# Optimization experiments

Hardware: AMD Instinct MI355X
Metric: run time of the kernel (lower is better)

The kernel has to match this reference:

```python
import jax, jax.numpy as jnp
import numpy as np

B, S, H, NH = 1, 4096, 768, 12
D = H // NH  # per-head dim = 64


def setup_inputs() -> dict:
    key = jax.random.key(0)
    ks = jax.random.split(key, 10)
    p = 0.02  # param scale
    return {
        "x": jax.random.normal(ks[0], (B, S, H), jnp.float32),
        "Wq": jax.random.normal(ks[1], (H, H), jnp.float32) * p,
        "bq": jax.random.normal(ks[2], (H,), jnp.float32) * p,
        "Wk": jax.random.normal(ks[3], (H, H), jnp.float32) * p,
        "bk": jax.random.normal(ks[4], (H,), jnp.float32) * p,
        "Wv": jax.random.normal(ks[5], (H, H), jnp.float32) * p,
        "bv": jax.random.normal(ks[6], (H,), jnp.float32) * p,
        "Wo": jax.random.normal(ks[7], (H, H), jnp.float32) * p,
        "bo": jax.random.normal(ks[8], (H,), jnp.float32) * p,
        "attn_mask": jax.random.randint(ks[9], (B, 1, 1, S), 0, 2).astype(bool),
    }


def _split_heads(t):
    # [B, S, H] -> [B, NH, S, D]
    return t.reshape(B, S, NH, D).transpose(0, 2, 1, 3)


def reference(x, Wq, bq, Wk, bk, Wv, bv, Wo, bo, attn_mask):
    q = _split_heads(x @ Wq.T + bq)
    k = _split_heads(x @ Wk.T + bk)
    v = _split_heads(x @ Wv.T + bv)
    scores = jnp.einsum('bhqd,bhkd->bhqk', q, k) / np.sqrt(D).astype(np.float32)
    scores = jnp.where(attn_mask, jnp.float32(-1e9), scores)
    attn = jax.nn.softmax(scores, axis=-1)
    ctx = jnp.einsum('bhqk,bhkd->bhqd', attn, v)
    ctx = ctx.transpose(0, 2, 1, 3).reshape(B, S, H)  # merge heads
    return ctx @ Wo.T + bo
```

## Files before the change

kernel.cpp:

```cpp
#include <hip/hip_runtime.h>
#include <stdint.h>

#define S_LEN 4096
#define HDIM  768
#define NHEAD 12
#define DHEAD 64

typedef _Float16 f16;
typedef __attribute__((ext_vector_type(8)))  _Float16 f16x8;
typedef __attribute__((ext_vector_type(4)))  _Float16 f16x4;
typedef __attribute__((ext_vector_type(4)))  float    f32x4;
typedef __attribute__((ext_vector_type(16))) float    f32x16;

typedef __attribute__((address_space(1))) void gv_t;
typedef __attribute__((address_space(3))) void lv_t;

__device__ __forceinline__ void async_copy16(const void* g, void* l) {
  __builtin_amdgcn_global_load_lds((gv_t*)g, (lv_t*)l, 16, 0, 0);
}

__device__ __forceinline__ float fast_exp2(float x) {
#if __has_builtin(__builtin_amdgcn_exp2f)
  return __builtin_amdgcn_exp2f(x);
#else
  return exp2f(x);
#endif
}

__device__ __forceinline__ int swz4(int row) { return (row ^ (row >> 2)) & 3; }

constexpr size_t OFF_META = 0;
constexpr size_t OFF_RIDX = 256;
constexpr size_t OFF_XB   = 65536;
constexpr size_t SZ_XB    = (size_t)S_LEN * HDIM * 2;
constexpr size_t OFF_WQKV = OFF_XB + SZ_XB;
constexpr size_t SZ_WQKV  = (size_t)3 * HDIM * HDIM * 2;
constexpr size_t OFF_WO   = OFF_WQKV + SZ_WQKV;
constexpr size_t SZ_WO    = (size_t)HDIM * HDIM * 2;
constexpr size_t OFF_Q    = OFF_WO + SZ_WO;
constexpr size_t SZ_HD    = (size_t)NHEAD * S_LEN * DHEAD * 2;
constexpr size_t OFF_K    = OFF_Q + SZ_HD;
constexpr size_t OFF_VT   = OFF_K + SZ_HD;
constexpr size_t OFF_VR   = OFF_VT + SZ_HD;
constexpr size_t OFF_PO1  = OFF_VR + SZ_HD;

__global__ __launch_bounds__(256) void k_prep(const float* __restrict__ x,
                                              const float* __restrict__ wq,
                                              const float* __restrict__ wk,
                                              const float* __restrict__ wv,
                                              const float* __restrict__ wo,
                                              const int* __restrict__ mi,
                                              f16* __restrict__ dst,
                                              int* __restrict__ ridx,
                                              int* __restrict__ meta) {
  __shared__ int s_flag;
  __shared__ int s_cnt[256];
  const int b = blockIdx.x, tid = threadIdx.x;
  if (b < 5376) {
    int i = b * 256 + tid;
    const float* src; int off;
    if (i < 786432) { src = x; off = i; }
    else {
      int j = i - 786432;
      int w = j / 147456;
      off = j - w * 147456;
      src = (w == 0) ? wq : (w == 1) ? wk : (w == 2) ? wv : wo;
    }
    float4 v = ((const float4*)src)[off];
    f16x4 h;
    h[0] = (f16)v.x; h[1] = (f16)v.y; h[2] = (f16)v.z; h[3] = (f16)v.w;
    ((f16x4*)dst)[i] = h;
    return;
  }
  if (tid == 0) s_flag = 1;
  __syncthreads();
  int bad = 0;
  #pragma unroll
  for (int k = 0; k < 4; ++k) {
    int v = mi[k * 256 + tid];
    if (v != 0 && v != 1) bad = 1;
  }
  if (bad) atomicAnd(&s_flag, 0);
  __syncthreads();
  const int isInt = s_flag;
  const unsigned char* mu8 = (const unsigned char*)mi;
  int keep[16]; int cnt = 0;
  const int s0 = tid * 16;
  #pragma unroll
  for (int k = 0; k < 16; ++k) {
    int mval = isInt ? mi[s0 + k] : (int)mu8[s0 + k];
    keep[k] = (mval == 0) ? 1 : 0;
    cnt += keep[k];
    ridx[s0 + k] = 0;
  }
  s_cnt[tid] = cnt;
  __syncthreads();
  for (int off = 1; off < 256; off <<= 1) {
    int t = (tid >= off) ? s_cnt[tid - off] : 0;
    __syncthreads();
    s_cnt[tid] += t;
    __syncthreads();
  }
  int base = s_cnt[tid] - cnt;
  #pragma unroll
  for (int k = 0; k < 16; ++k) {
    if (keep[k]) { ridx[base] = s0 + k; ++base; }
  }
  if (tid == 255) meta[0] = s_cnt[255];
}

__global__ __launch_bounds__(256) void k_qkv(
    const f16* __restrict__ xb, const f16* __restrict__ wqkv,
    const float* __restrict__ bq, const float* __restrict__ bk, const float* __restrict__ bv,
    const int* __restrict__ ridx, const int* __restrict__ meta,
    f16* __restrict__ Qh, f16* __restrict__ Kc, f16* __restrict__ Vrow) {
  __shared__ __attribute__((aligned(16))) f16 lA[128 * 32];
  __shared__ __attribute__((aligned(16))) f16 lB[128 * 32];
  const int tid = threadIdx.x;
  const int wid = tid >> 6, lane = tid & 63;
  const int hf = lane >> 5, l31 = lane & 31;
  const int wm = wid >> 1, wn = wid & 1;
  const int tn = blockIdx.x;
  const int m0 = blockIdx.y * 128;
  const int mat = tn / 6;
  const int nb = (tn % 6) * 128;
  const int kc = meta[0];
  if (mat != 0 && m0 >= kc) return;
  const f16* wbase = wqkv + (size_t)mat * HDIM * HDIM;

  const int ar0 = tid >> 2, ar1 = 64 + (tid >> 2);
  const f16* asrc0;
  const f16* asrc1;
  if (mat == 0) {
    asrc0 = xb + (size_t)(m0 + ar0) * HDIM;
    asrc1 = xb + (size_t)(m0 + ar1) * HDIM;
  } else {
    int g0 = (m0 + ar0 < kc) ? ridx[m0 + ar0] : 0;
    int g1 = (m0 + ar1 < kc) ? ridx[m0 + ar1] : 0;
    asrc0 = xb + (size_t)g0 * HDIM;
    asrc1 = xb + (size_t)g1 * HDIM;
  }
  const int slot = tid & 3;
  const int gs0 = slot ^ swz4(ar0);
  const int gs1 = slot ^ swz4(ar1);

  f32x16 acc[2][2] = {};

  for (int k0 = 0; k0 < HDIM; k0 += 32) {
    async_copy16((const char*)(asrc0 + k0) + gs0 * 16, (char*)lA + (wid * 64) * 16);
    async_copy16((const char*)(asrc1 + k0) + gs1 * 16, (char*)lA + (256 + wid * 64) * 16);
    async_copy16((const char*)(wbase + (size_t)(nb + ar0) * HDIM + k0) + gs0 * 16,
                 (char*)lB + (wid * 64) * 16);
    async_copy16((const char*)(wbase + (size_t)(nb + ar1) * HDIM + k0) + gs1 * 16,
                 (char*)lB + (256 + wid * 64) * 16);
    __syncthreads();
    #pragma unroll
    for (int kk = 0; kk < 2; ++kk) {
      f16x8 af[2], bf[2];
      #pragma unroll
      for (int mi = 0; mi < 2; ++mi) {
        int row = wm * 64 + mi * 32 + l31;
        af[mi] = *(const f16x8*)&lA[row * 32 + (((kk * 2 + hf) ^ swz4(row)) * 8)];
      }
      #pragma unroll
      for (int ni = 0; ni < 2; ++ni) {
        int row = wn * 64 + ni * 32 + l31;
        bf[ni] = *(const f16x8*)&lB[row * 32 + (((kk * 2 + hf) ^ swz4(row)) * 8)];
      }
      #pragma unroll
      for (int mi = 0; mi < 2; ++mi)
        #pragma unroll
        for (int ni = 0; ni < 2; ++ni)
          acc[mi][ni] = __builtin_amdgcn_mfma_f32_32x32x16_f16(af[mi], bf[ni], acc[mi][ni], 0, 0, 0);
    }
    __syncthreads();
  }

  const float* bias = (mat == 0) ? bq : (mat == 1) ? bk : bv;
  const float qscale = 0.125f * 1.44269504088896341f;
  f16* kvdst = (mat == 1) ? Kc : Vrow;
  #pragma unroll
  for (int mi = 0; mi < 2; ++mi) {
    #pragma unroll
    for (int ni = 0; ni < 2; ++ni) {
      int n = nb + wn * 64 + ni * 32 + l31;
      int head = n >> 6, d = n & 63;
      float b = bias[n];
      #pragma unroll
      for (int reg = 0; reg < 16; ++reg) {
        int s = m0 + wm * 64 + mi * 32 + (reg & 3) + 8 * (reg >> 2) + 4 * hf;
        float val = acc[mi][ni][reg] + b;
        if (mat == 0) {
          Qh[((size_t)head * S_LEN + s) * DHEAD + d] = (f16)(val * qscale);
        } else if (s < kc) {
          kvdst[((size_t)head * S_LEN + s) * DHEAD + d] = (f16)val;
        }
      }
    }
  }
}

__global__ __launch_bounds__(256) void k_vt(const int* __restrict__ meta,
                                            const f16* __restrict__ Vrow,
                                            f16* __restrict__ Vtc,
                                            f16* __restrict__ Kc) {
  const int kc = meta[0];
  const int kcp = (kc + 63) & ~63;
  const int p0 = blockIdx.x * 64;
  const int h = blockIdx.y;
  const int tid = threadIdx.x;
  if (p0 >= kcp) return;
  if (p0 <= kc && kc < p0 + 64 && kc < kcp) {
    const int npad = kcp - kc;
    for (int u = tid; u < npad * 8; u += 256) {
      int r = kc + (u >> 3), c8 = u & 7;
      f16x8 z = {};
      *(f16x8*)&Kc[((size_t)h * S_LEN + r) * DHEAD + c8 * 8] = z;
    }
  }
  __shared__ __attribute__((aligned(16))) f16 lT[64 * 80];
  for (int u = tid; u < 512; u += 256) {
    int d8 = u >> 6, p = u & 63;
    f16x8 v = {};
    if (p0 + p < kc) v = *(const f16x8*)&Vrow[((size_t)h * S_LEN + p0 + p) * DHEAD + d8 * 8];
    #pragma unroll
    for (int j = 0; j < 8; ++j) lT[(d8 * 8 + j) * 80 + p] = v[j];
  }
  __syncthreads();
  for (int w = tid; w < 512; w += 256) {
    int d = w >> 3, p8 = w & 7;
    int base16 = (p8 >> 1) * 16, half = p8 & 1;
    f16x4 lo = *(const f16x4*)&lT[d * 80 + base16 + half * 4];
    f16x4 hi = *(const f16x4*)&lT[d * 80 + base16 + 8 + half * 4];
    f16x8 o;
    o[0] = lo[0]; o[1] = lo[1]; o[2] = lo[2]; o[3] = lo[3];
    o[4] = hi[0]; o[5] = hi[1]; o[6] = hi[2]; o[7] = hi[3];
    *(f16x8*)&Vtc[((size_t)h * DHEAD + d) * S_LEN + p0 + p8 * 8] = o;
  }
}

__global__ __launch_bounds__(256, 3) void k_attn(
    const f16* __restrict__ Qh, const f16* __restrict__ Kc, const f16* __restrict__ Vtc,
    const int* __restrict__ meta, f16* __restrict__ PO0, f16* __restrict__ PO1,
    float* __restrict__ PL) {
  __shared__ __attribute__((aligned(16))) f16 lK[2][64 * 64];
  __shared__ __attribute__((aligned(16))) f16 lV[2][64 * 64];
  const int tid = threadIdx.x;
  const int wid = tid >> 6, lane = tid & 63;
  const int hf = lane >> 5, l31 = lane & 31, r7 = l31 & 7;

  const int lid = blockIdx.x;
  const int w = ((lid & 7) * 96) + (lid >> 3);
  const int head = w >> 6;
  const int rem = w & 63;
  const int split = rem >> 5;
  const int q0 = (rem & 31) * 128 + wid * 32;

  const int kc = meta[0];
  const int nkt = (kc + 63) >> 6;
  const int th = nkt >> 1;
  const int t0 = split ? th : 0;
  const int t1 = split ? nkt : th;

  const f16* Qp = Qh + ((size_t)head * S_LEN + q0 + l31) * DHEAD;
  f16x8 qf[4];
  #pragma unroll
  for (int dc = 0; dc < 4; ++dc) qf[dc] = *(const f16x8*)(Qp + dc * 16 + hf * 8);

  f32x16 accO[2] = {};
  float ls0 = 0.f, ls1 = 0.f, ls2 = 0.f, ls3 = 0.f;

  const char* kbase = (const char*)(Kc + (size_t)head * S_LEN * DHEAD);
  const char* vbase = (const char*)(Vtc + (size_t)head * DHEAD * S_LEN);

  const int c0row = tid >> 3,        c0slot = tid & 7;
  const int c1row = (256 + tid) >> 3, c1slot = tid & 7;
  const int gs0 = c0slot ^ (c0row & 7);
  const int gs1 = c1slot ^ (c1row & 7);

  auto stage = [&](int t, int buf) {
    const int j0 = t * 64;
    async_copy16(kbase + (size_t)(j0 + c0row) * 128 + gs0 * 16,
                 (char*)&lK[buf][0] + (wid * 64) * 16);
    async_copy16(vbase + (size_t)c0row * (S_LEN * 2) + (size_t)j0 * 2 + gs0 * 16,
                 (char*)&lV[buf][0] + (wid * 64) * 16);
    async_copy16(kbase + (size_t)(j0 + c1row) * 128 + gs1 * 16,
                 (char*)&lK[buf][0] + (256 + wid * 64) * 16);
    async_copy16(vbase + (size_t)c1row * (S_LEN * 2) + (size_t)j0 * 2 + gs1 * 16,
                 (char*)&lV[buf][0] + (256 + wid * 64) * 16);
  };

  int cur = 0;
  if (t0 < t1) {
    stage(t0, 0);
    __syncthreads();
  }

  for (int t = t0; t < t1; ++t) {
    const bool more = (t + 1 < t1);
    if (more) stage(t + 1, cur ^ 1);

    #pragma unroll
    for (int mh = 0; mh < 2; ++mh) {
      f16x8 af[4];
      const int arow = mh * 32 + l31;
      #pragma unroll
      for (int dc = 0; dc < 4; ++dc)
        af[dc] = *(const f16x8*)&lK[cur][arow * 64 + ((((dc << 1) | hf) ^ r7) * 8)];
      f32x16 s = {};
      #pragma unroll
      for (int dc = 0; dc < 4; ++dc)
        s = __builtin_amdgcn_mfma_f32_32x32x16_f16(af[dc], qf[dc], s, 0, 0, 0);
      #pragma unroll
      for (int u = 0; u < 16; ++u) {
        s[u] = fast_exp2(s[u]);
        if ((u & 3) == 0) ls0 += s[u];
        else if ((u & 3) == 1) ls1 += s[u];
        else if ((u & 3) == 2) ls2 += s[u];
        else ls3 += s[u];
      }
      #pragma unroll
      for (int cc = 0; cc < 2; ++cc) {
        f16x8 pf;
        #pragma unroll
        for (int u = 0; u < 8; ++u) pf[u] = (f16)s[8 * cc + u];
        const int c2 = mh * 2 + cc;
        #pragma unroll
        for (int dh = 0; dh < 2; ++dh) {
          const int vrow = dh * 32 + l31;
          f16x8 vf = *(const f16x8*)&lV[cur][vrow * 64 + ((((c2 << 1) | hf) ^ r7) * 8)];
          accO[dh] = __builtin_amdgcn_mfma_f32_32x32x16_f16(pf, vf, accO[dh], 0, 0, 0);
        }
      }
    }

    if (more) {
      __syncthreads();
      cur ^= 1;
    }
  }

  float lsum = (ls0 + ls1) + (ls2 + ls3);
  lsum += __shfl_xor(lsum, 32);
  if (split == 1) lsum -= (float)(nkt * 64 - kc);
  if (hf == 0)
    PL[((size_t)split * NHEAD + head) * S_LEN + q0 + l31] = lsum;

  f16* PO = split ? PO1 : PO0;
  #pragma unroll
  for (int dh = 0; dh < 2; ++dh)
    #pragma unroll
    for (int reg = 0; reg < 16; ++reg) {
      int row = (reg & 3) + 8 * (reg >> 2) + 4 * hf;
      PO[((size_t)head * S_LEN + q0 + row) * DHEAD + dh * 32 + l31] = (f16)accO[dh][reg];
    }
}

__global__ __launch_bounds__(256) void k_out(
    const f16* __restrict__ PO0, const f16* __restrict__ PO1,
    const float* __restrict__ PL, const f16* __restrict__ wo,
    const float* __restrict__ bo, float* __restrict__ out) {
  __shared__ __attribute__((aligned(16))) f16 lA[128 * 32];
  __shared__ __attribute__((aligned(16))) f16 lB[128 * 32];
  __shared__ float linv[NHEAD * 128];
  const int tid = threadIdx.x;
  const int wid = tid >> 6, lane = tid & 63;
  const int hf = lane >> 5, l31 = lane & 31;
  const int wm = wid >> 1, wn = wid & 1;
  const int nb = blockIdx.x * 128;
  const int m0 = blockIdx.y * 128;

  for (int i = tid; i < NHEAD * 128; i += 256) {
    int h = i >> 7, r = i & 127;
    float l = PL[(size_t)h * S_LEN + m0 + r] + PL[(size_t)(NHEAD + h) * S_LEN + m0 + r];
    linv[i] = 1.0f / l;
  }
  __syncthreads();

  f32x16 acc[2][2] = {};

  for (int k0 = 0; k0 < HDIM; k0 += 32) {
    const int head = k0 >> 6, d0 = k0 & 63;
    #pragma unroll
    for (int iss = 0; iss < 2; ++iss) {
      int c = iss * 256 + tid;
      int row = c >> 2, slot = c & 3;
      int gs = slot ^ swz4(row);
      size_t pi = ((size_t)head * S_LEN + m0 + row) * DHEAD + d0 + gs * 8;
      f16x8 a0 = *(const f16x8*)(PO0 + pi);
      f16x8 a1 = *(const f16x8*)(PO1 + pi);
      float il = linv[head * 128 + row];
      f16x8 av;
      #pragma unroll
      for (int u = 0; u < 8; ++u) av[u] = (f16)(((float)a0[u] + (float)a1[u]) * il);
      *(f16x8*)&lA[c * 8] = av;
      async_copy16((const char*)(wo + (size_t)(nb + row) * HDIM + k0) + gs * 16,
                   (char*)lB + (iss * 256 + wid * 64) * 16);
    }
    __syncthreads();
    #pragma unroll
    for (int kk = 0; kk < 2; ++kk) {
      f16x8 af[2], bf[2];
      #pragma unroll
      for (int mi = 0; mi < 2; ++mi) {
        int row = wm * 64 + mi * 32 + l31;
        af[mi] = *(const f16x8*)&lA[row * 32 + (((kk * 2 + hf) ^ swz4(row)) * 8)];
      }
      #pragma unroll
      for (int ni = 0; ni < 2; ++ni) {
        int row = wn * 64 + ni * 32 + l31;
        bf[ni] = *(const f16x8*)&lB[row * 32 + (((kk * 2 + hf) ^ swz4(row)) * 8)];
      }
      #pragma unroll
      for (int mi = 0; mi < 2; ++mi)
        #pragma unroll
        for (int ni = 0; ni < 2; ++ni)
          acc[mi][ni] = __builtin_amdgcn_mfma_f32_32x32x16_f16(af[mi], bf[ni], acc[mi][ni], 0, 0, 0);
    }
    __syncthreads();
  }

  #pragma unroll
  for (int mi = 0; mi < 2; ++mi) {
    #pragma unroll
    for (int ni = 0; ni < 2; ++ni) {
      int n = nb + wn * 64 + ni * 32 + l31;
      float b = bo[n];
      #pragma unroll
      for (int reg = 0; reg < 16; ++reg) {
        int s = m0 + wm * 64 + mi * 32 + (reg & 3) + 8 * (reg >> 2) + 4 * hf;
        out[(size_t)s * HDIM + n] = acc[mi][ni][reg] + b;
      }
    }
  }
}

extern "C" void kernel_launch(void* const* d_in, const int* in_sizes, int n_in,
                              void* d_out, int out_size, void* d_ws, size_t ws_size,
                              hipStream_t stream) {
  const float* x  = (const float*)d_in[0];
  const float* Wq = (const float*)d_in[1];
  const float* bq = (const float*)d_in[2];
  const float* Wk = (const float*)d_in[3];
  const float* bk = (const float*)d_in[4];
  const float* Wv = (const float*)d_in[5];
  const float* bv = (const float*)d_in[6];
  const float* Wo = (const float*)d_in[7];
  const float* bo = (const float*)d_in[8];
  const int*   mask = (const int*)d_in[9];
  float* out = (float*)d_out;

  char* ws = (char*)d_ws;
  int* meta  = (int*)(ws + OFF_META);
  int* ridx  = (int*)(ws + OFF_RIDX);
  f16* xb    = (f16*)(ws + OFF_XB);
  f16* wqkv  = (f16*)(ws + OFF_WQKV);
  f16* wob   = (f16*)(ws + OFF_WO);
  f16* Qh    = (f16*)(ws + OFF_Q);
  f16* Kc    = (f16*)(ws + OFF_K);
  f16* Vtc   = (f16*)(ws + OFF_VT);
  f16* Vrow  = (f16*)(ws + OFF_VR);
  f16* PO0   = (f16*)(ws + OFF_VR);
  f16* PO1   = (f16*)(ws + OFF_PO1);
  float* PL  = (float*)(ws + OFF_WQKV);

  k_prep<<<dim3(5377), 256, 0, stream>>>(x, Wq, Wk, Wv, Wo, mask, xb, ridx, meta);
  k_qkv<<<dim3(18, 32), 256, 0, stream>>>(xb, wqkv, bq, bk, bv, ridx, meta, Qh, Kc, Vrow);
  k_vt<<<dim3(64, NHEAD), 256, 0, stream>>>(meta, Vrow, Vtc, Kc);
  k_attn<<<dim3(768), 256, 0, stream>>>(Qh, Kc, Vtc, meta, PO0, PO1, PL);
  k_out<<<dim3(6, 32), 256, 0, stream>>>(PO0, PO1, PL, wob, bo, out);
}
```

Baseline: 178.2 us.

## Stage attention output via LDS for coalesced stores; retile output projection

The attention kernel now writes its per-wave output tile to shared memory, reusing the K buffer, and then stores it to global memory as 16-byte rows. Before, each lane wrote scattered 2-byte values. The output projection kernel moves from 128x128 tiles with a K-step of 32 to 128x64 tiles with a full head (64) per K-step. This doubles the grid to 384 blocks for better CU occupancy and halves the number of syncs per block. A swizzled 1-D block index groups blocks that share A rows. The trade-off is that the PO/linv normalization on A is now recomputed twice as many times across the N blocks.

```diff
diff --git a/kernel.cpp b/kernel.cpp
--- a/kernel.cpp
+++ b/kernel.cpp
@@ -273,7 +273,7 @@
   const char* kbase = (const char*)(Kc + (size_t)head * S_LEN * DHEAD);
   const char* vbase = (const char*)(Vtc + (size_t)head * DHEAD * S_LEN);
 
-  const int c0row = tid >> 3,        c0slot = tid & 7;
+  const int c0row = tid >> 3,         c0slot = tid & 7;
   const int c1row = (256 + tid) >> 3, c1slot = tid & 7;
   const int gs0 = c0slot ^ (c0row & 7);
   const int gs1 = c1slot ^ (c1row & 7);
@@ -346,29 +346,40 @@
   if (hf == 0)
     PL[((size_t)split * NHEAD + head) * S_LEN + q0 + l31] = lsum;
 
-  f16* PO = split ? PO1 : PO0;
+  __syncthreads();
+  f16* ost = (f16*)lK;
   #pragma unroll
   for (int dh = 0; dh < 2; ++dh)
     #pragma unroll
     for (int reg = 0; reg < 16; ++reg) {
       int row = (reg & 3) + 8 * (reg >> 2) + 4 * hf;
-      PO[((size_t)head * S_LEN + q0 + row) * DHEAD + dh * 32 + l31] = (f16)accO[dh][reg];
-    }
+      ost[wid * 2048 + row * 64 + dh * 32 + l31] = (f16)accO[dh][reg];
+    }
+  f16* PO = split ? PO1 : PO0;
+  const f16* osrc = ost + wid * 2048;
+  #pragma unroll
+  for (int p = 0; p < 4; ++p) {
+    int row = p * 8 + (lane >> 3), sl = lane & 7;
+    f16x8 v = *(const f16x8*)&osrc[row * 64 + sl * 8];
+    *(f16x8*)&PO[((size_t)head * S_LEN + q0 + row) * DHEAD + sl * 8] = v;
+  }
 }
 
 __global__ __launch_bounds__(256) void k_out(
     const f16* __restrict__ PO0, const f16* __restrict__ PO1,
     const float* __restrict__ PL, const f16* __restrict__ wo,
     const float* __restrict__ bo, float* __restrict__ out) {
-  __shared__ __attribute__((aligned(16))) f16 lA[128 * 32];
-  __shared__ __attribute__((aligned(16))) f16 lB[128 * 32];
+  __shared__ __attribute__((aligned(16))) f16 lA[128 * 64];
+  __shared__ __attribute__((aligned(16))) f16 lB[64 * 64];
   __shared__ float linv[NHEAD * 128];
   const int tid = threadIdx.x;
   const int wid = tid >> 6, lane = tid & 63;
   const int hf = lane >> 5, l31 = lane & 31;
   const int wm = wid >> 1, wn = wid & 1;
-  const int nb = blockIdx.x * 128;
-  const int m0 = blockIdx.y * 128;
+  const int lid = blockIdx.x;
+  const int w = ((lid & 7) * 48) + (lid >> 3);
+  const int nb = (w % 12) * 64;
+  const int m0 = (w / 12) * 128;
 
   for (int i = tid; i < NHEAD * 128; i += 256) {
     int h = i >> 7, r = i & 127;
@@ -377,16 +388,15 @@
   }
   __syncthreads();
 
-  f32x16 acc[2][2] = {};
-
-  for (int k0 = 0; k0 < HDIM; k0 += 32) {
-    const int head = k0 >> 6, d0 = k0 & 63;
-    #pragma unroll
-    for (int iss = 0; iss < 2; ++iss) {
-      int c = iss * 256 + tid;
-      int row = c >> 2, slot = c & 3;
-      int gs = slot ^ swz4(row);
-      size_t pi = ((size_t)head * S_LEN + m0 + row) * DHEAD + d0 + gs * 8;
+  f32x16 acc[2] = {};
+
+  for (int head = 0; head < NHEAD; ++head) {
+    #pragma unroll
+    for (int it = 0; it < 4; ++it) {
+      int c = it * 256 + tid;
+      int row = c >> 3, slot = c & 7;
+      int gs = slot ^ (row & 7);
+      size_t pi = ((size_t)head * S_LEN + m0 + row) * DHEAD + gs * 8;
       f16x8 a0 = *(const f16x8*)(PO0 + pi);
       f16x8 a1 = *(const f16x8*)(PO1 + pi);
       float il = linv[head * 128 + row];
@@ -394,43 +404,41 @@
       #pragma unroll
       for (int u = 0; u < 8; ++u) av[u] = (f16)(((float)a0[u] + (float)a1[u]) * il);
       *(f16x8*)&lA[c * 8] = av;
-      async_copy16((const char*)(wo + (size_t)(nb + row) * HDIM + k0) + gs * 16,
-                   (char*)lB + (iss * 256 + wid * 64) * 16);
-    }
-    __syncthreads();
-    #pragma unroll
-    for (int kk = 0; kk < 2; ++kk) {
-      f16x8 af[2], bf[2];
+    }
+    #pragma unroll
+    for (int it = 0; it < 2; ++it) {
+      int c = it * 256 + tid;
+      int row = c >> 3, slot = c & 7;
+      int gs = slot ^ (row & 7);
+      async_copy16((const char*)(wo + (size_t)(nb + row) * HDIM + head * 64) + gs * 16,
+                   (char*)lB + (it * 256 + wid * 64) * 16);
+    }
+    __syncthreads();
+    #pragma unroll
+    for (int kk = 0; kk < 4; ++kk) {
+      f16x8 af[2], bf;
       #pragma unroll
       for (int mi = 0; mi < 2; ++mi) {
         int row = wm * 64 + mi * 32 + l31;
-        af[mi] = *(const f16x8*)&lA[row * 32 + (((kk * 2 + hf) ^ swz4(row)) * 8)];
-      }
-      #pragma unroll
-      for (int ni = 0; ni < 2; ++ni) {
-        int row = wn * 64 + ni * 32 + l31;
-        bf[ni] = *(const f16x8*)&lB[row * 32 + (((kk * 2 + hf) ^ swz4(row)) * 8)];
-      }
+        af[mi] = *(const f16x8*)&lA[row * 64 + ((((kk << 1) | hf) ^ (row & 7)) * 8)];
+      }
+      int rb = wn * 32 + l31;
+      bf = *(const f16x8*)&lB[rb * 64 + ((((kk << 1) | hf) ^ (rb & 7)) * 8)];
       #pragma unroll
       for (int mi = 0; mi < 2; ++mi)
-        #pragma unroll
-        for (int ni = 0; ni < 2; ++ni)
-          acc[mi][ni] = __builtin_amdgcn_mfma_f32_32x32x16_f16(af[mi], bf[ni], acc[mi][ni], 0, 0, 0);
-    }
-    __syncthreads();
-  }
-
+        acc[mi] = __builtin_amdgcn_mfma_f32_32x32x16_f16(af[mi], bf, acc[mi], 0, 0, 0);
+    }
+    __syncthreads();
+  }
+
+  const int n = nb + wn * 32 + l31;
+  const float b = bo[n];
   #pragma unroll
   for (int mi = 0; mi < 2; ++mi) {
     #pragma unroll
-    for (int ni = 0; ni < 2; ++ni) {
-      int n = nb + wn * 64 + ni * 32 + l31;
-      float b = bo[n];
-      #pragma unroll
-      for (int reg = 0; reg < 16; ++reg) {
-        int s = m0 + wm * 64 + mi * 32 + (reg & 3) + 8 * (reg >> 2) + 4 * hf;
-        out[(size_t)s * HDIM + n] = acc[mi][ni][reg] + b;
-      }
+    for (int reg = 0; reg < 16; ++reg) {
+      int s = m0 + wm * 64 + mi * 32 + (reg & 3) + 8 * (reg >> 2) + 4 * hf;
+      out[(size_t)s * HDIM + n] = acc[mi][reg] + b;
     }
   }
 }
@@ -468,5 +476,5 @@
   k_qkv<<<dim3(18, 32), 256, 0, stream>>>(xb, wqkv, bq, bk, bv, ridx, meta, Qh, Kc, Vrow);
   k_vt<<<dim3(64, NHEAD), 256, 0, stream>>>(meta, Vrow, Vtc, Kc);
   k_attn<<<dim3(768), 256, 0, stream>>>(Qh, Kc, Vtc, meta, PO0, PO1, PL);
-  k_out<<<dim3(6, 32), 256, 0, stream>>>(PO0, PO1, PL, wob, bo, out);
-}
+  k_out<<<dim3(384), 256, 0, stream>>>(PO0, PO1, PL, wob, bo, out);
+}
```

Result: no change. 175.9 us (-1.3%).
